# Optimization experiments

Measured on AMD Instinct MI355X. Metric: run time of the kernel, lower is better.

The kernel has to match this reference:

```python
import jax, jax.numpy as jnp
import numpy as np

EMBED = 64
OUT = 64
KERW = 64
DIM = 3

def setup_inputs() -> dict:
    key = jax.random.key(0)
    ks = jax.random.split(key, 6)
    x = jax.random.normal(ks[0], (8, 4096, EMBED), dtype=jnp.float32)
    grid = jax.random.uniform(ks[1], (8, 4096, DIM), dtype=jnp.float32)
    # DenseNet([dim, ker_width_l, output_size*embed_size], GELU): two Linear layers,
    # GELU between, no activation after the last layer.
    W1 = jax.random.normal(ks[2], (DIM, KERW), dtype=jnp.float32) / np.sqrt(DIM)
    b1 = jnp.zeros((KERW,), dtype=jnp.float32)
    W2 = jax.random.normal(ks[3], (KERW, OUT * EMBED), dtype=jnp.float32) / np.sqrt(KERW)
    b2 = jnp.zeros((OUT * EMBED,), dtype=jnp.float32)
    return {"x": x, "grid": grid, "W1": W1, "b1": b1, "W2": W2, "b2": b2}

def reference(x, grid, W1, b1, W2, b2):
    shape = x.shape
    # generator MLP: grid [.., dim] -> per-point weight [.., embed*out]
    h = jax.nn.gelu(grid @ W1 + b1, approximate=False)
    weight = h @ W2 + b2                              # [B, P, embed*out]
    weight = weight.reshape(-1, EMBED, OUT)           # [N, embed, out]
    xf = x.reshape(-1, shape[-1])                     # [N, embed]
    out = jnp.einsum('bi,bio->bo', xf, weight)        # [N, out]
    return out.reshape(*shape[:-1], OUT)
```

## Files before the change

kernel.cpp:

```cpp
#include <hip/hip_runtime.h>
#include <hip/hip_bf16.h>
#include <hip/hip_fp16.h>

typedef _Float16 f16x8 __attribute__((ext_vector_type(8)));
typedef float f32x4 __attribute__((ext_vector_type(4)));

#define N_PTS 32768
#define NCHUNK 65
#define ROWS 64
#define H_STRIDE 72
#define X_STRIDE 72
#define P_STRIDE 68

__global__ __launch_bounds__(256) void prep_kernel(
    const float* __restrict__ W2, const float* __restrict__ b2,
    _Float16* __restrict__ wsB) {
  __shared__ _Float16 w_lds[64][X_STRIDE];
  const int c   = blockIdx.x;
  const int tid = threadIdx.x;
  {
    const float* src = (c < 64) ? (W2 + c * 4096 + tid * 16) : (b2 + tid * 16);
    int kl = tid >> 2, o = (tid & 3) * 16;
    f16x8 v0, v1;
    #pragma unroll
    for (int j = 0; j < 8; ++j) {
      v0[j] = (_Float16)src[j];
      v1[j] = (_Float16)src[8 + j];
    }
    *(f16x8*)(&w_lds[kl][o])     = v0;
    *(f16x8*)(&w_lds[kl][o + 8]) = v1;
  }
  __syncthreads();
  #pragma unroll
  for (int u = 0; u < 2; ++u) {
    int t = tid + u * 256;
    int q = t >> 6, lane = t & 63;
    int klbase = (q >> 2) * 32 + ((lane >> 4) & 3) * 8;
    int o      = (q & 3) * 16 + (lane & 15);
    f16x8 v;
    #pragma unroll
    for (int j = 0; j < 8; ++j) v[j] = w_lds[klbase + j][o];
    *(f16x8*)(wsB + c * 4096 + t * 8) = v;
  }
}

__global__ __launch_bounds__(256) void main_kernel(
    const float* __restrict__ x, const float* __restrict__ gridp,
    const float* __restrict__ W1, const float* __restrict__ b1,
    const _Float16* __restrict__ wsB, float* __restrict__ out) {

  __shared__ _Float16 h_lds[ROWS][H_STRIDE];
  __shared__ float part[4][ROWS * P_STRIDE];
  _Float16* x_lds = (_Float16*)&part[0][0];

  const int tid  = threadIdx.x;
  const int lane = tid & 63;
  const int wave = tid >> 6;
  const int rowblk = blockIdx.x * ROWS;

  const float* xsrc = x + rowblk * 64 + tid * 16;
  f32x4 xr0 = *(const f32x4*)(xsrc);
  f32x4 xr1 = *(const f32x4*)(xsrc + 4);
  f32x4 xr2 = *(const f32x4*)(xsrc + 8);
  f32x4 xr3 = *(const f32x4*)(xsrc + 12);

  {
    int row = tid >> 2;
    int kb  = (tid & 3) * 16;
    int r = rowblk + row;
    float g0 = gridp[r * 3 + 0], g1 = gridp[r * 3 + 1], g2 = gridp[r * 3 + 2];
    f16x8 h0, h1;
    #pragma unroll
    for (int q = 0; q < 16; ++q) {
      int k = kb + q;
      float v = g0 * W1[k] + g1 * W1[64 + k] + g2 * W1[128 + k] + b1[k];
      float h = 0.5f * v * (1.0f + erff(v * 0.7071067811865476f));
      if (q < 8) h0[q] = (_Float16)h; else h1[q - 8] = (_Float16)h;
    }
    *(f16x8*)(&h_lds[row][kb])     = h0;
    *(f16x8*)(&h_lds[row][kb + 8]) = h1;
    if ((tid & 3) == 3) h_lds[row][64] = (_Float16)1.0f;
  }

  {
    int row = tid >> 2, o = (tid & 3) * 16;
    f16x8 v0, v1;
    #pragma unroll
    for (int j = 0; j < 4; ++j) {
      v0[j]     = (_Float16)xr0[j];
      v0[4 + j] = (_Float16)xr1[j];
      v1[j]     = (_Float16)xr2[j];
      v1[4 + j] = (_Float16)xr3[j];
    }
    *(f16x8*)(&x_lds[row * X_STRIDE + o])     = v0;
    *(f16x8*)(&x_lds[row * X_STRIDE + o + 8]) = v1;
  }
  __syncthreads();

  const int mrow = lane & 15;
  const int kgrp = lane >> 4;

  const _Float16* bp = wsB + lane * 8;

  auto LOADB = [&](f16x8* b, int c) {
    #pragma unroll
    for (int q = 0; q < 8; ++q)
      b[q] = *(const f16x8*)(bp + (c * 8 + q) * 512);
  };

  f16x8 bufA[8], bufB[8];
  LOADB(bufA, wave);

  f16x8 xf[4][2];
  #pragma unroll
  for (int m = 0; m < 4; ++m)
    #pragma unroll
    for (int s = 0; s < 2; ++s)
      xf[m][s] = *(const f16x8*)(&x_lds[(m * 16 + mrow) * X_STRIDE + s * 32 + kgrp * 8]);

  f32x4 acc[4][4];
  #pragma unroll
  for (int m = 0; m < 4; ++m)
    #pragma unroll
    for (int n = 0; n < 4; ++n)
      acc[m][n] = (f32x4){0.f, 0.f, 0.f, 0.f};

  auto COMPUTE = [&](const f16x8* b, int c) {
    #pragma unroll
    for (int m = 0; m < 4; ++m) {
      _Float16 hh = h_lds[m * 16 + mrow][c];
      f16x8 hs = {hh, hh, hh, hh, hh, hh, hh, hh};
      f16x8 a0 = xf[m][0] * hs;
      f16x8 a1 = xf[m][1] * hs;
      #pragma unroll
      for (int n = 0; n < 4; ++n) {
        acc[m][n] = __builtin_amdgcn_mfma_f32_16x16x32_f16(a0, b[n],     acc[m][n], 0, 0, 0);
        acc[m][n] = __builtin_amdgcn_mfma_f32_16x16x32_f16(a1, b[4 + n], acc[m][n], 0, 0, 0);
      }
    }
  };

  const int nch = (wave == 0) ? 17 : 16;
  int i = 1;
  for (; i + 1 < nch; i += 2) {
    LOADB(bufB, wave + 4 * i);
    COMPUTE(bufA, wave + 4 * (i - 1));
    LOADB(bufA, wave + 4 * (i + 1));
    COMPUTE(bufB, wave + 4 * i);
  }
  if (i < nch) {
    LOADB(bufB, wave + 4 * i);
    COMPUTE(bufA, wave + 4 * (i - 1));
    COMPUTE(bufB, wave + 4 * i);
  } else {
    COMPUTE(bufA, wave + 4 * (nch - 1));
  }

  __syncthreads();

  {
    float* pw = part[wave];
    #pragma unroll
    for (int m = 0; m < 4; ++m)
      #pragma unroll
      for (int n = 0; n < 4; ++n)
        #pragma unroll
        for (int r = 0; r < 4; ++r)
          pw[(m * 16 + kgrp * 4 + r) * P_STRIDE + n * 16 + mrow] = acc[m][n][r];
  }
  __syncthreads();

  {
    int row = tid >> 2;
    int cb  = (tid & 3) * 16;
    const float* p0 = part[0] + row * P_STRIDE + cb;
    float* op = out + (rowblk + row) * 64 + cb;
    #pragma unroll
    for (int j = 0; j < 4; ++j) {
      f32x4 s = *(const f32x4*)(p0 + j * 4);
      #pragma unroll
      for (int w = 1; w < 4; ++w)
        s += *(const f32x4*)(p0 + w * (ROWS * P_STRIDE) + j * 4);
      *(f32x4*)(op + j * 4) = s;
    }
  }
}

extern "C" void kernel_launch(void* const* d_in, const int* in_sizes, int n_in,
                              void* d_out, int out_size, void* d_ws, size_t ws_size,
                              hipStream_t stream) {
  const float* x    = (const float*)d_in[0];
  const float* grid = (const float*)d_in[1];
  const float* W1   = (const float*)d_in[2];
  const float* b1   = (const float*)d_in[3];
  const float* W2   = (const float*)d_in[4];
  const float* b2   = (const float*)d_in[5];
  float* out = (float*)d_out;
  _Float16* wsB = (_Float16*)d_ws;

  hipLaunchKernelGGL(prep_kernel, dim3(NCHUNK), dim3(256), 0, stream,
                     W2, b2, wsB);
  hipLaunchKernelGGL(main_kernel, dim3(N_PTS / ROWS), dim3(256), 0, stream,
                     x, grid, W1, b1, wsB, out);
}
```

Before: 33.09 us.

## Triple-buffer B-chunk loads and special-case bias chunk without h scaling

Replaces the double-buffered chunk loop with a fully unrolled triple-buffered pipeline, so each wave keeps two chunk loads in flight while computing on the third. The per-chunk h values are prefetched into registers alongside the B fragments, which takes LDS reads out of the compute body. The bias chunk (index 64) is handled by a dedicated path that skips the multiply by h, so the constant-1 column in h_lds is no longer written. This costs more vector registers (three 8-vector buffers), which can lower occupancy.

```diff
diff --git a/kernel.cpp b/kernel.cpp
--- a/kernel.cpp
+++ b/kernel.cpp
@@ -3,6 +3,7 @@
 #include <hip/hip_fp16.h>
 
 typedef _Float16 f16x8 __attribute__((ext_vector_type(8)));
+typedef _Float16 f16x4v __attribute__((ext_vector_type(4)));
 typedef float f32x4 __attribute__((ext_vector_type(4)));
 
 #define N_PTS 32768
@@ -79,7 +80,6 @@
     }
     *(f16x8*)(&h_lds[row][kb])     = h0;
     *(f16x8*)(&h_lds[row][kb + 8]) = h1;
-    if ((tid & 3) == 3) h_lds[row][64] = (_Float16)1.0f;
   }
 
   {
@@ -107,9 +107,18 @@
     for (int q = 0; q < 8; ++q)
       b[q] = *(const f16x8*)(bp + (c * 8 + q) * 512);
   };
-
-  f16x8 bufA[8], bufB[8];
-  LOADB(bufA, wave);
+  auto LOADH = [&](int c) -> f16x4v {
+    f16x4v h;
+    #pragma unroll
+    for (int m = 0; m < 4; ++m) h[m] = h_lds[m * 16 + mrow][c];
+    return h;
+  };
+
+  f16x8 bA[8], bB[8], bC[8];
+  f16x4v ha, hb, hc;
+  LOADB(bA, wave);      ha = LOADH(wave);
+  LOADB(bB, wave + 4);  hb = LOADH(wave + 4);
+  LOADB(bC, wave + 8);  hc = LOADH(wave + 8);
 
   f16x8 xf[4][2];
   #pragma unroll
@@ -125,10 +134,10 @@
     for (int n = 0; n < 4; ++n)
       acc[m][n] = (f32x4){0.f, 0.f, 0.f, 0.f};
 
-  auto COMPUTE = [&](const f16x8* b, int c) {
+  auto COMPUTE = [&](const f16x8* b, f16x4v hv) {
     #pragma unroll
     for (int m = 0; m < 4; ++m) {
-      _Float16 hh = h_lds[m * 16 + mrow][c];
+      _Float16 hh = hv[m];
       f16x8 hs = {hh, hh, hh, hh, hh, hh, hh, hh};
       f16x8 a0 = xf[m][0] * hs;
       f16x8 a1 = xf[m][1] * hs;
@@ -139,22 +148,28 @@
       }
     }
   };
-
-  const int nch = (wave == 0) ? 17 : 16;
-  int i = 1;
-  for (; i + 1 < nch; i += 2) {
-    LOADB(bufB, wave + 4 * i);
-    COMPUTE(bufA, wave + 4 * (i - 1));
-    LOADB(bufA, wave + 4 * (i + 1));
-    COMPUTE(bufB, wave + 4 * i);
-  }
-  if (i < nch) {
-    LOADB(bufB, wave + 4 * i);
-    COMPUTE(bufA, wave + 4 * (i - 1));
-    COMPUTE(bufB, wave + 4 * i);
-  } else {
-    COMPUTE(bufA, wave + 4 * (nch - 1));
-  }
+  auto COMPUTE_BIAS = [&](const f16x8* b) {
+    #pragma unroll
+    for (int m = 0; m < 4; ++m)
+      #pragma unroll
+      for (int n = 0; n < 4; ++n) {
+        acc[m][n] = __builtin_amdgcn_mfma_f32_16x16x32_f16(xf[m][0], b[n],     acc[m][n], 0, 0, 0);
+        acc[m][n] = __builtin_amdgcn_mfma_f32_16x16x32_f16(xf[m][1], b[4 + n], acc[m][n], 0, 0, 0);
+      }
+  };
+
+  #pragma unroll
+  for (int g = 0; g < 5; ++g) {
+    COMPUTE(bA, ha);
+    if (3 * g + 3 < 16) { LOADB(bA, wave + 4 * (3 * g + 3)); ha = LOADH(wave + 4 * (3 * g + 3)); }
+    COMPUTE(bB, hb);
+    if (3 * g + 4 < 16) { LOADB(bB, wave + 4 * (3 * g + 4)); hb = LOADH(wave + 4 * (3 * g + 4)); }
+    else if (wave == 0) { LOADB(bB, 64); }
+    COMPUTE(bC, hc);
+    if (3 * g + 5 < 16) { LOADB(bC, wave + 4 * (3 * g + 5)); hc = LOADH(wave + 4 * (3 * g + 5)); }
+  }
+  COMPUTE(bA, ha);
+  if (wave == 0) COMPUTE_BIAS(bB);
 
   __syncthreads();
 
```

New measurement: 31.90 us. 3.6% less time.

## Partition rows across waves with LDS-staged double-buffered weight chunks

Applied to the files above, without the earlier changes.

Each block now covers 128 rows and each wave owns 32 rows over all K chunks, which removes the cross-wave partial-sum reduction through LDS. The prepared W2 chunks are staged cooperatively into a double-buffered LDS area, with global prefetch overlapped with MFMA compute. Chunk order is rotated per block to spread L2 traffic, and the bias chunk is applied as a final MFMA pass. In exchange the block needs more LDS and a barrier per chunk pair, and the grid has half as many blocks.

```diff
diff --git a/kernel.cpp b/kernel.cpp
--- a/kernel.cpp
+++ b/kernel.cpp
@@ -7,15 +7,13 @@
 
 #define N_PTS 32768
 #define NCHUNK 65
-#define ROWS 64
+#define ROWS_BLK 128
 #define H_STRIDE 72
-#define X_STRIDE 72
-#define P_STRIDE 68
 
 __global__ __launch_bounds__(256) void prep_kernel(
     const float* __restrict__ W2, const float* __restrict__ b2,
     _Float16* __restrict__ wsB) {
-  __shared__ _Float16 w_lds[64][X_STRIDE];
+  __shared__ _Float16 w_lds[64][H_STRIDE];
   const int c   = blockIdx.x;
   const int tid = threadIdx.x;
   {
@@ -49,86 +47,97 @@
     const float* __restrict__ W1, const float* __restrict__ b1,
     const _Float16* __restrict__ wsB, float* __restrict__ out) {
 
-  __shared__ _Float16 h_lds[ROWS][H_STRIDE];
-  __shared__ float part[4][ROWS * P_STRIDE];
-  _Float16* x_lds = (_Float16*)&part[0][0];
+  __shared__ _Float16 bbuf[2][8192];
+  __shared__ _Float16 biasb[4096];
+  __shared__ _Float16 h_lds[ROWS_BLK][H_STRIDE];
 
   const int tid  = threadIdx.x;
   const int lane = tid & 63;
   const int wave = tid >> 6;
-  const int rowblk = blockIdx.x * ROWS;
-
-  const float* xsrc = x + rowblk * 64 + tid * 16;
-  f32x4 xr0 = *(const f32x4*)(xsrc);
-  f32x4 xr1 = *(const f32x4*)(xsrc + 4);
-  f32x4 xr2 = *(const f32x4*)(xsrc + 8);
-  f32x4 xr3 = *(const f32x4*)(xsrc + 12);
-
-  {
-    int row = tid >> 2;
-    int kb  = (tid & 3) * 16;
+  const int rowblk = blockIdx.x * ROWS_BLK;
+  const int rot = blockIdx.x & 31;
+  const int mrow = lane & 15;
+  const int kgrp = lane >> 4;
+
+  const char* wsb = (const char*)wsB;
+  auto pidx = [&](int s) { return (s + rot) & 31; };
+
+  f32x4 st[4], sb[2];
+  {
+    int p0 = pidx(0);
+    #pragma unroll
+    for (int i = 0; i < 4; ++i)
+      st[i] = *(const f32x4*)(wsb + p0 * 16384 + (wave + 4 * i) * 1024 + lane * 16);
+    #pragma unroll
+    for (int i = 0; i < 2; ++i)
+      sb[i] = *(const f32x4*)(wsb + 64 * 8192 + (wave + 4 * i) * 1024 + lane * 16);
+  }
+
+  f32x4 xr[2][2][2];
+  #pragma unroll
+  for (int m = 0; m < 2; ++m)
+    #pragma unroll
+    for (int s = 0; s < 2; ++s) {
+      const float* xp = x + (rowblk + wave * 32 + m * 16 + mrow) * 64 + s * 32 + kgrp * 8;
+      xr[m][s][0] = *(const f32x4*)(xp);
+      xr[m][s][1] = *(const f32x4*)(xp + 4);
+    }
+
+  {
+    int row = tid >> 1, half = tid & 1;
     int r = rowblk + row;
     float g0 = gridp[r * 3 + 0], g1 = gridp[r * 3 + 1], g2 = gridp[r * 3 + 2];
-    f16x8 h0, h1;
-    #pragma unroll
-    for (int q = 0; q < 16; ++q) {
-      int k = kb + q;
-      float v = g0 * W1[k] + g1 * W1[64 + k] + g2 * W1[128 + k] + b1[k];
-      float h = 0.5f * v * (1.0f + erff(v * 0.7071067811865476f));
-      if (q < 8) h0[q] = (_Float16)h; else h1[q - 8] = (_Float16)h;
-    }
-    *(f16x8*)(&h_lds[row][kb])     = h0;
-    *(f16x8*)(&h_lds[row][kb + 8]) = h1;
-    if ((tid & 3) == 3) h_lds[row][64] = (_Float16)1.0f;
-  }
-
-  {
-    int row = tid >> 2, o = (tid & 3) * 16;
-    f16x8 v0, v1;
-    #pragma unroll
-    for (int j = 0; j < 4; ++j) {
-      v0[j]     = (_Float16)xr0[j];
-      v0[4 + j] = (_Float16)xr1[j];
-      v1[j]     = (_Float16)xr2[j];
-      v1[4 + j] = (_Float16)xr3[j];
-    }
-    *(f16x8*)(&x_lds[row * X_STRIDE + o])     = v0;
-    *(f16x8*)(&x_lds[row * X_STRIDE + o + 8]) = v1;
-  }
+    #pragma unroll
+    for (int kb = 0; kb < 32; kb += 8) {
+      f16x8 hv;
+      #pragma unroll
+      for (int q = 0; q < 8; ++q) {
+        int k = half * 32 + kb + q;
+        float v = g0 * W1[k] + g1 * W1[64 + k] + g2 * W1[128 + k] + b1[k];
+        hv[q] = (_Float16)(0.5f * v * (1.0f + erff(v * 0.7071067811865476f)));
+      }
+      *(f16x8*)(&h_lds[row][half * 32 + kb]) = hv;
+    }
+  }
+
+  f16x8 xf[2][2];
+  #pragma unroll
+  for (int m = 0; m < 2; ++m)
+    #pragma unroll
+    for (int s = 0; s < 2; ++s) {
+      f16x8 v;
+      #pragma unroll
+      for (int j = 0; j < 4; ++j) {
+        v[j]     = (_Float16)xr[m][s][0][j];
+        v[4 + j] = (_Float16)xr[m][s][1][j];
+      }
+      xf[m][s] = v;
+    }
+
+  #pragma unroll
+  for (int i = 0; i < 4; ++i)
+    *(f32x4*)((char*)&bbuf[0][0] + (wave + 4 * i) * 1024 + lane * 16) = st[i];
+  #pragma unroll
+  for (int i = 0; i < 2; ++i)
+    *(f32x4*)((char*)&biasb[0] + (wave + 4 * i) * 1024 + lane * 16) = sb[i];
   __syncthreads();
 
-  const int mrow = lane & 15;
-  const int kgrp = lane >> 4;
-
-  const _Float16* bp = wsB + lane * 8;
-
-  auto LOADB = [&](f16x8* b, int c) {
-    #pragma unroll
-    for (int q = 0; q < 8; ++q)
-      b[q] = *(const f16x8*)(bp + (c * 8 + q) * 512);
-  };
-
-  f16x8 bufA[8], bufB[8];
-  LOADB(bufA, wave);
-
-  f16x8 xf[4][2];
-  #pragma unroll
-  for (int m = 0; m < 4; ++m)
-    #pragma unroll
-    for (int s = 0; s < 2; ++s)
-      xf[m][s] = *(const f16x8*)(&x_lds[(m * 16 + mrow) * X_STRIDE + s * 32 + kgrp * 8]);
-
-  f32x4 acc[4][4];
-  #pragma unroll
-  for (int m = 0; m < 4; ++m)
+  f32x4 acc[2][4];
+  #pragma unroll
+  for (int m = 0; m < 2; ++m)
     #pragma unroll
     for (int n = 0; n < 4; ++n)
       acc[m][n] = (f32x4){0.f, 0.f, 0.f, 0.f};
 
+  auto FRAGS = [&](const _Float16* buf, int ch, f16x8* b) {
+    #pragma unroll
+    for (int q = 0; q < 8; ++q)
+      b[q] = *(const f16x8*)(buf + ch * 4096 + q * 512 + lane * 8);
+  };
   auto COMPUTE = [&](const f16x8* b, int c) {
     #pragma unroll
-    for (int m = 0; m < 4; ++m) {
-      _Float16 hh = h_lds[m * 16 + mrow][c];
+    for (int m = 0; m < 2; ++m) {
+      _Float16 hh = h_lds[wave * 32 + m * 16 + mrow][c];
       f16x8 hs = {hh, hh, hh, hh, hh, hh, hh, hh};
       f16x8 a0 = xf[m][0] * hs;
       f16x8 a1 = xf[m][1] * hs;
@@ -140,50 +149,68 @@
     }
   };
 
-  const int nch = (wave == 0) ? 17 : 16;
-  int i = 1;
-  for (; i + 1 < nch; i += 2) {
-    LOADB(bufB, wave + 4 * i);
-    COMPUTE(bufA, wave + 4 * (i - 1));
-    LOADB(bufA, wave + 4 * (i + 1));
-    COMPUTE(bufB, wave + 4 * i);
-  }
-  if (i < nch) {
-    LOADB(bufB, wave + 4 * i);
-    COMPUTE(bufA, wave + 4 * (i - 1));
-    COMPUTE(bufB, wave + 4 * i);
-  } else {
-    COMPUTE(bufA, wave + 4 * (nch - 1));
-  }
-
-  __syncthreads();
-
-  {
-    float* pw = part[wave];
-    #pragma unroll
-    for (int m = 0; m < 4; ++m)
-      #pragma unroll
-      for (int n = 0; n < 4; ++n)
+  for (int t = 0; t < 16; ++t) {
+    {
+      int pn = pidx(2 * t + 1);
+      f32x4 stg[4];
+      #pragma unroll
+      for (int i = 0; i < 4; ++i)
+        stg[i] = *(const f32x4*)(wsb + pn * 16384 + (wave + 4 * i) * 1024 + lane * 16);
+      int c0 = 2 * pidx(2 * t);
+      f16x8 b0[8], b1[8];
+      FRAGS(bbuf[0], 0, b0);
+      FRAGS(bbuf[0], 1, b1);
+      COMPUTE(b0, c0);
+      COMPUTE(b1, c0 + 1);
+      #pragma unroll
+      for (int i = 0; i < 4; ++i)
+        *(f32x4*)((char*)&bbuf[1][0] + (wave + 4 * i) * 1024 + lane * 16) = stg[i];
+      __syncthreads();
+    }
+    {
+      int c0 = 2 * pidx(2 * t + 1);
+      f32x4 stg[4];
+      if (t < 15) {
+        int pn = pidx(2 * t + 2);
         #pragma unroll
-        for (int r = 0; r < 4; ++r)
-          pw[(m * 16 + kgrp * 4 + r) * P_STRIDE + n * 16 + mrow] = acc[m][n][r];
-  }
-  __syncthreads();
-
-  {
-    int row = tid >> 2;
-    int cb  = (tid & 3) * 16;
-    const float* p0 = part[0] + row * P_STRIDE + cb;
-    float* op = out + (rowblk + row) * 64 + cb;
-    #pragma unroll
-    for (int j = 0; j < 4; ++j) {
-      f32x4 s = *(const f32x4*)(p0 + j * 4);
-      #pragma unroll
-      for (int w = 1; w < 4; ++w)
-        s += *(const f32x4*)(p0 + w * (ROWS * P_STRIDE) + j * 4);
-      *(f32x4*)(op + j * 4) = s;
-    }
-  }
+        for (int i = 0; i < 4; ++i)
+          stg[i] = *(const f32x4*)(wsb + pn * 16384 + (wave + 4 * i) * 1024 + lane * 16);
+      }
+      f16x8 b0[8], b1[8];
+      FRAGS(bbuf[1], 0, b0);
+      FRAGS(bbuf[1], 1, b1);
+      COMPUTE(b0, c0);
+      COMPUTE(b1, c0 + 1);
+      if (t < 15) {
+        #pragma unroll
+        for (int i = 0; i < 4; ++i)
+          *(f32x4*)((char*)&bbuf[0][0] + (wave + 4 * i) * 1024 + lane * 16) = stg[i];
+        __syncthreads();
+      }
+    }
+  }
+
+  {
+    f16x8 bb[8];
+    FRAGS(biasb, 0, bb);
+    #pragma unroll
+    for (int m = 0; m < 2; ++m)
+      #pragma unroll
+      for (int n = 0; n < 4; ++n) {
+        acc[m][n] = __builtin_amdgcn_mfma_f32_16x16x32_f16(xf[m][0], bb[n],     acc[m][n], 0, 0, 0);
+        acc[m][n] = __builtin_amdgcn_mfma_f32_16x16x32_f16(xf[m][1], bb[4 + n], acc[m][n], 0, 0, 0);
+      }
+  }
+
+  #pragma unroll
+  for (int m = 0; m < 2; ++m)
+    #pragma unroll
+    for (int n = 0; n < 4; ++n) {
+      int row = rowblk + wave * 32 + m * 16 + kgrp * 4;
+      #pragma unroll
+      for (int r = 0; r < 4; ++r)
+        out[(row + r) * 64 + n * 16 + mrow] = acc[m][n][r];
+    }
 }
 
 extern "C" void kernel_launch(void* const* d_in, const int* in_sizes, int n_in,
@@ -200,6 +227,6 @@
 
   hipLaunchKernelGGL(prep_kernel, dim3(NCHUNK), dim3(256), 0, stream,
                      W2, b2, wsB);
-  hipLaunchKernelGGL(main_kernel, dim3(N_PTS / ROWS), dim3(256), 0, stream,
+  hipLaunchKernelGGL(main_kernel, dim3(N_PTS / ROWS_BLK), dim3(256), 0, stream,
                      x, grid, W1, b1, wsB, out);
 }
```

Result: slower. 38.67 us (+16.9%).

## Split waves over output columns and stage weight chunks in LDS

Applied to the files above, without the earlier changes.

The main kernel now divides work among waves by output columns instead of by hidden chunks. All 65 weight chunks are streamed into a shared double-buffered LDS area with global_load_lds, and every wave reads its slice from there. This removes the per-wave partial-sum buffer and the cross-wave reduction, and it frees a large amount of LDS, which should allow more blocks per CU. x is now loaded straight from global memory into MFMA fragments, and the bias chunk is handled as a separate final step. In exchange the loop needs a block barrier on every chunk, and the code depends on the asynchronous LDS loads being complete before each barrier.

```diff
diff --git a/kernel.cpp b/kernel.cpp
--- a/kernel.cpp
+++ b/kernel.cpp
@@ -9,13 +9,11 @@
 #define NCHUNK 65
 #define ROWS 64
 #define H_STRIDE 72
-#define X_STRIDE 72
-#define P_STRIDE 68
 
 __global__ __launch_bounds__(256) void prep_kernel(
     const float* __restrict__ W2, const float* __restrict__ b2,
     _Float16* __restrict__ wsB) {
-  __shared__ _Float16 w_lds[64][X_STRIDE];
+  __shared__ _Float16 w_lds[64][H_STRIDE];
   const int c   = blockIdx.x;
   const int tid = threadIdx.x;
   {
@@ -49,20 +47,30 @@
     const float* __restrict__ W1, const float* __restrict__ b1,
     const _Float16* __restrict__ wsB, float* __restrict__ out) {
 
+  __shared__ _Float16 bbuf[2][4096];
   __shared__ _Float16 h_lds[ROWS][H_STRIDE];
-  __shared__ float part[4][ROWS * P_STRIDE];
-  _Float16* x_lds = (_Float16*)&part[0][0];
 
   const int tid  = threadIdx.x;
   const int lane = tid & 63;
   const int wave = tid >> 6;
   const int rowblk = blockIdx.x * ROWS;
+  const int mrow = lane & 15;
+  const int kgrp = lane >> 4;
 
-  const float* xsrc = x + rowblk * 64 + tid * 16;
-  f32x4 xr0 = *(const f32x4*)(xsrc);
-  f32x4 xr1 = *(const f32x4*)(xsrc + 4);
-  f32x4 xr2 = *(const f32x4*)(xsrc + 8);
-  f32x4 xr3 = *(const f32x4*)(xsrc + 12);
+  const char* wsb = (const char*)wsB;
+
+  auto STAGE = [&](int c, int par) {
+    const char* src = wsb + c * 8192 + wave * 1024 + lane * 16;
+    char* dst = (char*)&bbuf[par][0] + wave * 1024;
+    __builtin_amdgcn_global_load_lds(
+        (const __attribute__((address_space(1))) void*)src,
+        (__attribute__((address_space(3))) void*)dst, 16, 0, 0);
+    __builtin_amdgcn_global_load_lds(
+        (const __attribute__((address_space(1))) void*)(src + 4096),
+        (__attribute__((address_space(3))) void*)(dst + 4096), 16, 0, 0);
+  };
+
+  STAGE(0, 0);
 
   {
     int row = tid >> 2;
@@ -79,110 +87,63 @@
     }
     *(f16x8*)(&h_lds[row][kb])     = h0;
     *(f16x8*)(&h_lds[row][kb + 8]) = h1;
-    if ((tid & 3) == 3) h_lds[row][64] = (_Float16)1.0f;
   }
-
-  {
-    int row = tid >> 2, o = (tid & 3) * 16;
-    f16x8 v0, v1;
-    #pragma unroll
-    for (int j = 0; j < 4; ++j) {
-      v0[j]     = (_Float16)xr0[j];
-      v0[4 + j] = (_Float16)xr1[j];
-      v1[j]     = (_Float16)xr2[j];
-      v1[4 + j] = (_Float16)xr3[j];
-    }
-    *(f16x8*)(&x_lds[row * X_STRIDE + o])     = v0;
-    *(f16x8*)(&x_lds[row * X_STRIDE + o + 8]) = v1;
-  }
-  __syncthreads();
-
-  const int mrow = lane & 15;
-  const int kgrp = lane >> 4;
-
-  const _Float16* bp = wsB + lane * 8;
-
-  auto LOADB = [&](f16x8* b, int c) {
-    #pragma unroll
-    for (int q = 0; q < 8; ++q)
-      b[q] = *(const f16x8*)(bp + (c * 8 + q) * 512);
-  };
-
-  f16x8 bufA[8], bufB[8];
-  LOADB(bufA, wave);
 
   f16x8 xf[4][2];
   #pragma unroll
   for (int m = 0; m < 4; ++m)
     #pragma unroll
-    for (int s = 0; s < 2; ++s)
-      xf[m][s] = *(const f16x8*)(&x_lds[(m * 16 + mrow) * X_STRIDE + s * 32 + kgrp * 8]);
-
-  f32x4 acc[4][4];
-  #pragma unroll
-  for (int m = 0; m < 4; ++m)
-    #pragma unroll
-    for (int n = 0; n < 4; ++n)
-      acc[m][n] = (f32x4){0.f, 0.f, 0.f, 0.f};
-
-  auto COMPUTE = [&](const f16x8* b, int c) {
-    #pragma unroll
-    for (int m = 0; m < 4; ++m) {
-      _Float16 hh = h_lds[m * 16 + mrow][c];
-      f16x8 hs = {hh, hh, hh, hh, hh, hh, hh, hh};
-      f16x8 a0 = xf[m][0] * hs;
-      f16x8 a1 = xf[m][1] * hs;
+    for (int s = 0; s < 2; ++s) {
+      const float* xp = x + (rowblk + m * 16 + mrow) * 64 + s * 32 + kgrp * 8;
+      f32x4 a = *(const f32x4*)(xp);
+      f32x4 b = *(const f32x4*)(xp + 4);
+      f16x8 v;
       #pragma unroll
-      for (int n = 0; n < 4; ++n) {
-        acc[m][n] = __builtin_amdgcn_mfma_f32_16x16x32_f16(a0, b[n],     acc[m][n], 0, 0, 0);
-        acc[m][n] = __builtin_amdgcn_mfma_f32_16x16x32_f16(a1, b[4 + n], acc[m][n], 0, 0, 0);
+      for (int j = 0; j < 4; ++j) {
+        v[j]     = (_Float16)a[j];
+        v[4 + j] = (_Float16)b[j];
       }
+      xf[m][s] = v;
     }
-  };
-
-  const int nch = (wave == 0) ? 17 : 16;
-  int i = 1;
-  for (; i + 1 < nch; i += 2) {
-    LOADB(bufB, wave + 4 * i);
-    COMPUTE(bufA, wave + 4 * (i - 1));
-    LOADB(bufA, wave + 4 * (i + 1));
-    COMPUTE(bufB, wave + 4 * i);
-  }
-  if (i < nch) {
-    LOADB(bufB, wave + 4 * i);
-    COMPUTE(bufA, wave + 4 * (i - 1));
-    COMPUTE(bufB, wave + 4 * i);
-  } else {
-    COMPUTE(bufA, wave + 4 * (nch - 1));
-  }
 
   __syncthreads();
 
-  {
-    float* pw = part[wave];
+  f32x4 acc[4];
+  #pragma unroll
+  for (int m = 0; m < 4; ++m) acc[m] = (f32x4){0.f, 0.f, 0.f, 0.f};
+
+  for (int t = 0; t < 64; ++t) {
+    STAGE(t + 1, (t + 1) & 1);
+    const _Float16* bb = &bbuf[t & 1][0];
+    f16x8 bf0 = *(const f16x8*)(bb + (wave)     * 512 + lane * 8);
+    f16x8 bf1 = *(const f16x8*)(bb + (4 + wave) * 512 + lane * 8);
     #pragma unroll
-    for (int m = 0; m < 4; ++m)
-      #pragma unroll
-      for (int n = 0; n < 4; ++n)
-        #pragma unroll
-        for (int r = 0; r < 4; ++r)
-          pw[(m * 16 + kgrp * 4 + r) * P_STRIDE + n * 16 + mrow] = acc[m][n][r];
+    for (int m = 0; m < 4; ++m) {
+      _Float16 hh = h_lds[m * 16 + mrow][t];
+      f16x8 hs = {hh, hh, hh, hh, hh, hh, hh, hh};
+      acc[m] = __builtin_amdgcn_mfma_f32_16x16x32_f16(xf[m][0] * hs, bf0, acc[m], 0, 0, 0);
+      acc[m] = __builtin_amdgcn_mfma_f32_16x16x32_f16(xf[m][1] * hs, bf1, acc[m], 0, 0, 0);
+    }
+    __syncthreads();
   }
-  __syncthreads();
 
   {
-    int row = tid >> 2;
-    int cb  = (tid & 3) * 16;
-    const float* p0 = part[0] + row * P_STRIDE + cb;
-    float* op = out + (rowblk + row) * 64 + cb;
+    const _Float16* bb = &bbuf[0][0];
+    f16x8 bf0 = *(const f16x8*)(bb + (wave)     * 512 + lane * 8);
+    f16x8 bf1 = *(const f16x8*)(bb + (4 + wave) * 512 + lane * 8);
     #pragma unroll
-    for (int j = 0; j < 4; ++j) {
-      f32x4 s = *(const f32x4*)(p0 + j * 4);
-      #pragma unroll
-      for (int w = 1; w < 4; ++w)
-        s += *(const f32x4*)(p0 + w * (ROWS * P_STRIDE) + j * 4);
-      *(f32x4*)(op + j * 4) = s;
+    for (int m = 0; m < 4; ++m) {
+      acc[m] = __builtin_amdgcn_mfma_f32_16x16x32_f16(xf[m][0], bf0, acc[m], 0, 0, 0);
+      acc[m] = __builtin_amdgcn_mfma_f32_16x16x32_f16(xf[m][1], bf1, acc[m], 0, 0, 0);
     }
+  }
+
+  #pragma unroll
+  for (int m = 0; m < 4; ++m) {
+    int row = rowblk + m * 16 + kgrp * 4;
+    #pragma unroll
+    for (int r = 0; r < 4; ++r)
+      out[(row + r) * 64 + wave * 16 + mrow] = acc[m][r];
   }
 }
 
```

New measurement: 46.74 us. 41.2% more time.
